# Optimization experiments

Hardware: AMD Instinct MI355X
Metric: run time of the kernel (lower is better)

Reference implementation:

```python
import jax, jax.numpy as jnp
import numpy as np

EPS = 1e-6

def _ln(x, g, b):
    mu = jnp.mean(x, axis=-1, keepdims=True)
    var = jnp.mean(jnp.square(x - mu), axis=-1, keepdims=True)
    return (x - mu) * jax.lax.rsqrt(var + EPS) * g + b

def setup_inputs() -> dict:
    key = jax.random.key(0)
    ks = jax.random.split(key, 8)
    B, S, D, H, HD, F = 4, 1024, 1024, 16, 64, 4096
    s = 0.02
    return {
        "hidden_state": jax.random.normal(ks[0], (B, S, D), jnp.float32),
        "mask": jnp.ones((B, S), jnp.int32),
        "Wq": jax.random.normal(ks[1], (H, D, HD), jnp.float32) * s,
        "bq": jnp.zeros((H, HD), jnp.float32),
        "Wk": jax.random.normal(ks[2], (H, D, HD), jnp.float32) * s,
        "bk": jnp.zeros((H, HD), jnp.float32),
        "Wv": jax.random.normal(ks[3], (H, D, HD), jnp.float32) * s,
        "bv": jnp.zeros((H, HD), jnp.float32),
        "Wo": jax.random.normal(ks[4], (D, D), jnp.float32) * s,
        "bo": jnp.zeros((D,), jnp.float32),
        "ln1_g": jnp.ones((D,), jnp.float32),
        "ln1_b": jnp.zeros((D,), jnp.float32),
        "ln2_g": jnp.ones((D,), jnp.float32),
        "ln2_b": jnp.zeros((D,), jnp.float32),
        "W1": jax.random.normal(ks[5], (D, F), jnp.float32) * s,
        "b1": jnp.zeros((F,), jnp.float32),
        "W2": jax.random.normal(ks[6], (F, D), jnp.float32) * s,
        "b2": jnp.zeros((D,), jnp.float32),
    }

def reference(hidden_state, mask, Wq, bq, Wk, bk, Wv, bv, Wo, bo,
              ln1_g, ln1_b, ln2_g, ln2_b, W1, b1, W2, b2):
    # Pre-norm
    x1 = _ln(hidden_state, ln1_g, ln1_b)  # [B,S,D]
    # Per-head projections stacked over head axis h
    q = jnp.einsum('bsd,hdk->bhsk', x1, Wq) + bq[:, None, :]
    k = jnp.einsum('bsd,hdk->bhsk', x1, Wk) + bk[:, None, :]
    v = jnp.einsum('bsd,hdk->bhsk', x1, Wv) + bv[:, None, :]
    head_dim = q.shape[-1]
    scores = jnp.einsum('bhqk,bhsk->bhqs', q, k) / jnp.sqrt(jnp.float32(head_dim))
    scores = jnp.where(mask[:, None, None, :] == 0, jnp.float32(-1e9), scores)
    w = jax.nn.softmax(scores, axis=-1)
    attn = jnp.einsum('bhqs,bhsk->bhqk', w, v)  # [B,H,S,HD]
    B, H, S, HD = attn.shape
    attn = attn.transpose(0, 2, 1, 3).reshape(B, S, H * HD)  # concat heads
    attn = attn @ Wo + bo
    h = attn + hidden_state
    x2 = _ln(h, ln2_g, ln2_b)
    ff = jax.nn.gelu(x2 @ W1 + b1, approximate=False) @ W2 + b2
    return ff + h
```

## Files before the change

### kernel.cpp

```cpp
#include <hip/hip_runtime.h>

typedef __bf16 bf16;
typedef __bf16 bf16x4 __attribute__((ext_vector_type(4)));
typedef __bf16 bf16x8 __attribute__((ext_vector_type(8)));
typedef float  f32x4  __attribute__((ext_vector_type(4)));

#define F32X4_ZERO ((f32x4){0.f, 0.f, 0.f, 0.f})

__device__ __forceinline__ f32x4 mfma16(bf16x8 a, bf16x8 b, f32x4 c) {
  return __builtin_amdgcn_mfma_f32_16x16x32_bf16(a, b, c, 0, 0, 0);
}

__device__ __forceinline__ void gld16(const void* g, void* l) {
  __builtin_amdgcn_global_load_lds((const __attribute__((address_space(1))) void*)g,
                                   (__attribute__((address_space(3))) void*)l, 16, 0, 0);
}

__device__ __forceinline__ float gelu_f(float u) {
  return 0.5f * u * (1.0f + erff(u * 0.70710678118654752f));
}

__device__ __forceinline__ bf16x8 frag_ld(const bf16* base, int row, int c16) {
  return *(const bf16x8*)((const char*)base + row * 128 + (((c16) ^ (row & 7)) << 4));
}

__device__ __forceinline__ bf16x8 frag_ld32(const bf16* base, int row, int c16) {
  return *(const bf16x8*)((const char*)base + row * 64 + ((c16 ^ ((row >> 1) & 3)) << 4));
}
#define WAITB(N) asm volatile("s_waitcnt vmcnt(" #N ")\ns_barrier" ::: "memory")

__global__ void transpose2(const float* __restrict__ src, size_t sBatch, int sStride,
                           bf16* __restrict__ dst, size_t dBatch, int dStride) {
  __shared__ bf16 t[32][33];
  src += (size_t)blockIdx.z * sBatch;
  dst += (size_t)blockIdx.z * dBatch;
  int c0 = blockIdx.x * 32, r0 = blockIdx.y * 32;
#pragma unroll
  for (int i = 0; i < 4; i++) {
    int r = threadIdx.y + i * 8;
    t[r][threadIdx.x] = (bf16)src[(size_t)(r0 + r) * sStride + c0 + threadIdx.x];
  }
  __syncthreads();
#pragma unroll
  for (int i = 0; i < 4; i++) {
    int c = threadIdx.y + i * 8;
    dst[(size_t)(c0 + c) * dStride + r0 + threadIdx.x] = t[threadIdx.x][c];
  }
}

__global__ __launch_bounds__(256) void ln_rows(const float* __restrict__ in,
                                               const float* __restrict__ gam,
                                               const float* __restrict__ bet,
                                               bf16* __restrict__ out) {
  int row = blockIdx.x, tid = threadIdx.x;
  f32x4 x = *(const f32x4*)(in + (size_t)row * 1024 + tid * 4);
  float s = 0.f, q = 0.f;
#pragma unroll
  for (int j = 0; j < 4; j++) { s += x[j]; q += x[j] * x[j]; }
#pragma unroll
  for (int o = 1; o < 64; o <<= 1) {
    s += __shfl_xor(s, o, 64);
    q += __shfl_xor(q, o, 64);
  }
  __shared__ float red[8];
  if ((tid & 63) == 0) { red[(tid >> 6) * 2] = s; red[(tid >> 6) * 2 + 1] = q; }
  __syncthreads();
  s = red[0] + red[2] + red[4] + red[6];
  q = red[1] + red[3] + red[5] + red[7];
  float mean = s * (1.f / 1024.f);
  float var  = q * (1.f / 1024.f) - mean * mean;
  float inv  = rsqrtf(var + 1e-6f);
  bf16x4 o;
#pragma unroll
  for (int j = 0; j < 4; j++) {
    int c = tid * 4 + j;
    o[j] = (bf16)((x[j] - mean) * inv * gam[c] + bet[c]);
  }
  *(bf16x4*)(out + (size_t)row * 1024 + tid * 4) = o;
}

enum { EPI_WO = 0, EPI_GELU = 1, EPI_ACC0 = 2, EPI_ACC = 3, EPI_FINAL = 4 };

__global__ __launch_bounds__(512) void pipe256x128_gelu(
    const bf16* __restrict__ A, const bf16* __restrict__ BT, const float* __restrict__ bias,
    int N, bf16* __restrict__ outb) {
  int tid = threadIdx.x, lane = tid & 63, wv = tid >> 6;
  int bid = blockIdx.x;
  int xcd = bid & 7, idx = bid >> 3;
  int mg = xcd >> 1, ng = xcd & 1;
  int m0 = (mg * 4 + (idx >> 4)) * 256;
  int n0 = (ng * 16 + (idx & 15)) * 128;
  int wrow = (wv >> 1) * 64, wcol = (wv & 1) * 64;
  __shared__ __align__(16) bf16 lds[3][12288];
  f32x4 acc[4][4];
#pragma unroll
  for (int a = 0; a < 4; a++)
#pragma unroll
    for (int n = 0; n < 4; n++) acc[a][n] = F32X4_ZERO;

  constexpr int K = 1024, nk = K / 32;
  int rin = lane >> 2;
  int sbc = ((lane & 3) ^ ((lane >> 3) & 3)) * 16;
  auto stage = [&](int slot, int k0) {
#pragma unroll
    for (int j = 0; j < 3; j++) {
      int c = wv * 3 + j;
      if (c < 16)
        gld16((const char*)A + ((size_t)(m0 + c * 16 + rin) * K + k0) * 2 + sbc,
              (char*)lds[slot] + c * 1024);
      else
        gld16((const char*)BT + ((size_t)(n0 + (c - 16) * 16 + rin) * K + k0) * 2 + sbc,
              (char*)lds[slot] + c * 1024);
    }
  };

  stage(0, 0); stage(1, 32);
#pragma unroll 1
  for (int t = 0; t < nk; t++) {
    if (t < nk - 1) WAITB(3);
    else            WAITB(0);
    if (t + 2 < nk) stage((t + 2) % 3, (t + 2) * 32);
    const bf16* As = lds[t % 3];
    const bf16* Bs = lds[t % 3] + 8192;
    int c16 = lane >> 4;
    bf16x8 af[4], bfr[4];
#pragma unroll
    for (int mf = 0; mf < 4; mf++)
      af[mf] = frag_ld32(As, wrow + mf * 16 + (lane & 15), c16);
#pragma unroll
    for (int nf = 0; nf < 4; nf++)
      bfr[nf] = frag_ld32(Bs, wcol + nf * 16 + (lane & 15), c16);
#pragma unroll
    for (int mf = 0; mf < 4; mf++)
#pragma unroll
      for (int nf = 0; nf < 4; nf++)
        acc[mf][nf] = mfma16(af[mf], bfr[nf], acc[mf][nf]);
  }
#pragma unroll
  for (int mf = 0; mf < 4; mf++)
#pragma unroll
    for (int nf = 0; nf < 4; nf++)
#pragma unroll
      for (int i = 0; i < 4; i++) {
        int row = m0 + wrow + mf * 16 + ((lane >> 4) << 2) + i;
        int col = n0 + wcol + nf * 16 + (lane & 15);
        outb[(size_t)row * N + col] = (bf16)gelu_f(acc[mf][nf][i] + bias[col]);
      }
}

template <int EPI, int K, int NTL>
__global__ __launch_bounds__(256) void pipe128(
    const bf16* __restrict__ A, const bf16* __restrict__ BT, const float* __restrict__ bias,
    int N,
    const float* __restrict__ resid, float* __restrict__ facc,
    bf16* __restrict__ outb, float* __restrict__ outf) {
  int tid = threadIdx.x, lane = tid & 63, wv = tid >> 6;
  int bid = blockIdx.x + (blockIdx.y << 3);
  int xcd = bid & 7, idx = bid >> 3;
  int m0 = (xcd * 4 + (idx >> NTL)) * 128;
  int n0 = (idx & ((1 << NTL) - 1)) * 128;
  int wrow = (wv >> 1) * 64, wcol = (wv & 1) * 64;
  __shared__ __align__(16) bf16 lds[3][8192];
  f32x4 acc[4][4];
#pragma unroll
  for (int a = 0; a < 4; a++)
#pragma unroll
    for (int n = 0; n < 4; n++) acc[a][n] = F32X4_ZERO;

  constexpr int nk = K / 32;
  int rin = lane >> 2;
  int sbc = ((lane & 3) ^ ((lane >> 3) & 3)) * 16;
  auto stage = [&](int slot, int k0) {
#pragma unroll
    for (int j = 0; j < 4; j++) {
      int c = wv * 4 + j;
      if (c < 8)
        gld16((const char*)A + ((size_t)(m0 + c * 16 + rin) * K + k0) * 2 + sbc,
              (char*)lds[slot] + c * 1024);
      else
        gld16((const char*)BT + ((size_t)(n0 + (c - 8) * 16 + rin) * K + k0) * 2 + sbc,
              (char*)lds[slot] + c * 1024);
    }
  };

  stage(0, 0); stage(1, 32);
#pragma unroll 1
  for (int t = 0; t < nk; t++) {
    if (t < nk - 1) WAITB(4);
    else            WAITB(0);
    if (t + 2 < nk) stage((t + 2) % 3, (t + 2) * 32);
    const bf16* As = lds[t % 3];
    const bf16* Bs = lds[t % 3] + 4096;
    int c16 = lane >> 4;
    bf16x8 af[4], bfr[4];
#pragma unroll
    for (int mf = 0; mf < 4; mf++)
      af[mf] = frag_ld32(As, wrow + mf * 16 + (lane & 15), c16);
#pragma unroll
    for (int nf = 0; nf < 4; nf++)
      bfr[nf] = frag_ld32(Bs, wcol + nf * 16 + (lane & 15), c16);
#pragma unroll
    for (int mf = 0; mf < 4; mf++)
#pragma unroll
      for (int nf = 0; nf < 4; nf++)
        acc[mf][nf] = mfma16(af[mf], bfr[nf], acc[mf][nf]);
  }
#pragma unroll
  for (int mf = 0; mf < 4; mf++)
#pragma unroll
    for (int nf = 0; nf < 4; nf++)
#pragma unroll
      for (int i = 0; i < 4; i++) {
        int row = m0 + wrow + mf * 16 + ((lane >> 4) << 2) + i;
        int col = n0 + wcol + nf * 16 + (lane & 15);
        size_t idx2 = (size_t)row * N + col;
        float v = acc[mf][nf][i];
        if constexpr (EPI == EPI_WO) {
          outf[idx2] = v + bias[col] + resid[idx2];
        } else if constexpr (EPI == EPI_GELU) {
          outb[idx2] = (bf16)gelu_f(v + bias[col]);
        } else if constexpr (EPI == EPI_ACC0) {
          facc[idx2] = v;
        } else if constexpr (EPI == EPI_ACC) {
          facc[idx2] += v;
        } else {
          outf[idx2] = facc[idx2] + v + bias[col] + resid[idx2];
        }
      }
}

template <int KSTRIDE, int KLOOP, int NTL>
__global__ __launch_bounds__(256) void pipe128_part(
    const bf16* __restrict__ Abase, const bf16* __restrict__ BTbase,
    int N, bf16* __restrict__ p0, bf16* __restrict__ p1) {
  int tid = threadIdx.x, lane = tid & 63, wv = tid >> 6;
  int z = blockIdx.z;
  const bf16* A  = Abase  + (size_t)z * KLOOP;
  const bf16* BT = BTbase + (size_t)z * KLOOP;
  bf16* outp = z ? p1 : p0;
  int bid = blockIdx.x + (blockIdx.y << 3);
  int xcd = bid & 7, idx = bid >> 3;
  int m0 = (xcd * 4 + (idx >> NTL)) * 128;
  int n0 = (idx & ((1 << NTL) - 1)) * 128;
  int wrow = (wv >> 1) * 64, wcol = (wv & 1) * 64;
  __shared__ __align__(16) bf16 lds[3][8192];
  f32x4 acc[4][4];
#pragma unroll
  for (int a = 0; a < 4; a++)
#pragma unroll
    for (int n = 0; n < 4; n++) acc[a][n] = F32X4_ZERO;

  constexpr int nk = KLOOP / 32;
  int rin = lane >> 2;
  int sbc = ((lane & 3) ^ ((lane >> 3) & 3)) * 16;
  auto stage = [&](int slot, int k0) {
#pragma unroll
    for (int j = 0; j < 4; j++) {
      int c = wv * 4 + j;
      if (c < 8)
        gld16((const char*)A + ((size_t)(m0 + c * 16 + rin) * KSTRIDE + k0) * 2 + sbc,
              (char*)lds[slot] + c * 1024);
      else
        gld16((const char*)BT + ((size_t)(n0 + (c - 8) * 16 + rin) * KSTRIDE + k0) * 2 + sbc,
              (char*)lds[slot] + c * 1024);
    }
  };

  stage(0, 0); stage(1, 32);
#pragma unroll 1
  for (int t = 0; t < nk; t++) {
    if (t < nk - 1) WAITB(4);
    else            WAITB(0);
    if (t + 2 < nk) stage((t + 2) % 3, (t + 2) * 32);
    const bf16* As = lds[t % 3];
    const bf16* Bs = lds[t % 3] + 4096;
    int c16 = lane >> 4;
    bf16x8 af[4], bfr[4];
#pragma unroll
    for (int mf = 0; mf < 4; mf++)
      af[mf] = frag_ld32(As, wrow + mf * 16 + (lane & 15), c16);
#pragma unroll
    for (int nf = 0; nf < 4; nf++)
      bfr[nf] = frag_ld32(Bs, wcol + nf * 16 + (lane & 15), c16);
#pragma unroll
    for (int mf = 0; mf < 4; mf++)
#pragma unroll
      for (int nf = 0; nf < 4; nf++)
        acc[mf][nf] = mfma16(af[mf], bfr[nf], acc[mf][nf]);
  }
#pragma unroll
  for (int mf = 0; mf < 4; mf++)
#pragma unroll
    for (int nf = 0; nf < 4; nf++)
#pragma unroll
      for (int i = 0; i < 4; i++) {
        int row = m0 + wrow + mf * 16 + ((lane >> 4) << 2) + i;
        int col = n0 + wcol + nf * 16 + (lane & 15);
        outp[(size_t)row * N + col] = (bf16)acc[mf][nf][i];
      }
}

__global__ __launch_bounds__(256) void combine_k(
    const bf16* __restrict__ p0, const bf16* __restrict__ p1,
    const float* __restrict__ bias, const float* __restrict__ resid,
    float* __restrict__ out) {
  size_t i4 = ((size_t)blockIdx.x * 256 + threadIdx.x) * 4;
  bf16x4 a = *(const bf16x4*)(p0 + i4);
  bf16x4 b = *(const bf16x4*)(p1 + i4);
  f32x4 r = *(const f32x4*)(resid + i4);
  f32x4 bb = *(const f32x4*)(bias + (i4 & 1023));
  f32x4 o;
#pragma unroll
  for (int j = 0; j < 4; j++) o[j] = (float)a[j] + (float)b[j] + bb[j] + r[j];
  *(f32x4*)(out + i4) = o;
}

__global__ __launch_bounds__(256) void qkv_pipe(
    const bf16* __restrict__ x1,
    const bf16* __restrict__ WqT, const bf16* __restrict__ WkT, const bf16* __restrict__ WvT,
    const float* __restrict__ bq, const float* __restrict__ bk, const float* __restrict__ bv,
    bf16* __restrict__ qo, bf16* __restrict__ ko, bf16* __restrict__ vto) {
  int tid = threadIdx.x, lane = tid & 63, wv = tid >> 6;
  int z = blockIdx.z;
  const bf16* BT; const float* bias;
  if (z == 0)      { BT = WqT; bias = bq; }
  else if (z == 1) { BT = WkT; bias = bk; }
  else             { BT = WvT; bias = bv; }
  int bid = blockIdx.x + (blockIdx.y << 3);
  int xcd = bid & 7, idx = bid >> 3;
  int m0 = (xcd * 4 + (idx >> 3)) * 128, n0 = (idx & 7) * 128;
  int wrow = (wv >> 1) * 64, wcol = (wv & 1) * 64;
  __shared__ __align__(16) bf16 lds[3][8192];
  f32x4 acc[4][4];
#pragma unroll
  for (int a = 0; a < 4; a++)
#pragma unroll
    for (int n = 0; n < 4; n++) acc[a][n] = F32X4_ZERO;

  constexpr int K = 1024, nk = K / 32;
  int rin = lane >> 2;
  int sbc = ((lane & 3) ^ ((lane >> 3) & 3)) * 16;
  auto stage = [&](int slot, int k0) {
#pragma unroll
    for (int j = 0; j < 4; j++) {
      int c = wv * 4 + j;
      if (c < 8)
        gld16((const char*)x1 + ((size_t)(m0 + c * 16 + rin) * K + k0) * 2 + sbc,
              (char*)lds[slot] + c * 1024);
      else
        gld16((const char*)BT + ((size_t)(n0 + (c - 8) * 16 + rin) * K + k0) * 2 + sbc,
              (char*)lds[slot] + c * 1024);
    }
  };

  stage(0, 0); stage(1, 32);
#pragma unroll 1
  for (int t = 0; t < nk; t++) {
    if (t < nk - 1) WAITB(4);
    else            WAITB(0);
    if (t + 2 < nk) stage((t + 2) % 3, (t + 2) * 32);
    const bf16* As = lds[t % 3];
    const bf16* Bs = lds[t % 3] + 4096;
    int c16 = lane >> 4;
    bf16x8 af[4], bfr[4];
#pragma unroll
    for (int mf = 0; mf < 4; mf++)
      af[mf] = frag_ld32(As, wrow + mf * 16 + (lane & 15), c16);
#pragma unroll
    for (int nf = 0; nf < 4; nf++)
      bfr[nf] = frag_ld32(Bs, wcol + nf * 16 + (lane & 15), c16);
#pragma unroll
    for (int mf = 0; mf < 4; mf++)
#pragma unroll
      for (int nf = 0; nf < 4; nf++)
        acc[mf][nf] = mfma16(af[mf], bfr[nf], acc[mf][nf]);
  }
#pragma unroll
  for (int mf = 0; mf < 4; mf++)
#pragma unroll
    for (int nf = 0; nf < 4; nf++)
#pragma unroll
      for (int i = 0; i < 4; i++) {
        int row  = m0 + wrow + mf * 16 + ((lane >> 4) << 2) + i;
        int ncol = n0 + wcol + nf * 16 + (lane & 15);
        int bb = row >> 10, s = row & 1023, head = ncol >> 6, d = ncol & 63;
        size_t bh = (size_t)bb * 16 + head;
        float v = acc[mf][nf][i] + bias[ncol];
        if (z == 0)      qo[(bh * 1024 + s) * 64 + d] = (bf16)(v * 0.125f);
        else if (z == 1) ko[(bh * 1024 + s) * 64 + d] = (bf16)v;
        else             vto[(bh * 64 + d) * 1024 + s] = (bf16)v;
      }
}

__global__ __launch_bounds__(512) void attn_flash(
    const bf16* __restrict__ qb, const bf16* __restrict__ kb, const bf16* __restrict__ vtb,
    const int* __restrict__ mask, bf16* __restrict__ attnC) {
  int tid = threadIdx.x, lane = tid & 63, wv = tid >> 6;
  int wgid = blockIdx.x;
  int nid  = (wgid & 7) * 64 + (wgid >> 3);
  int qblk = nid & 7, h = (nid >> 3) & 15, b = nid >> 7;
  int qrow0 = qblk * 128 + wv * 16;

  __shared__ float smask[1024];
  __shared__ __align__(16) bf16 kt[2][64 * 64];
  __shared__ __align__(16) bf16 vt[2][64 * 64];
  __shared__ __align__(16) bf16 pb[8][16][72];
  for (int i = tid; i < 1024; i += 512) smask[i] = mask[b * 1024 + i] ? 0.f : -1e9f;

  size_t bh = (size_t)b * 16 + h;
  const bf16* qp = qb + (bh * 1024 + qrow0) * 64;
  bf16x8 qa[2];
#pragma unroll
  for (int kc = 0; kc < 2; kc++)
    qa[kc] = *(const bf16x8*)(qp + (lane & 15) * 64 + kc * 32 + (lane >> 4) * 8);

  const bf16* kp = kb + bh * 1024 * 64;
  const bf16* vp = vtb + bh * 64 * 1024;
  bf16* myp = &pb[wv][0][0];

  bf16x8 vone;
#pragma unroll
  for (int j = 0; j < 8; j++) vone[j] = (bf16)1.0f;

  f32x4 ssum = F32X4_ZERO;
  f32x4 oacc[4];
#pragma unroll
  for (int i = 0; i < 4; i++) oacc[i] = F32X4_ZERO;

  int srl = lane >> 3;
  int sbc = ((lane & 7) ^ srl) * 16;
  auto stage = [&](int buf, int t2) {
    int key0n = t2 * 64;
#pragma unroll
    for (int j = 0; j < 2; j++) {
      int c = wv * 2 + j;
      if (c < 8) {
        int row = c * 8 + srl;
        gld16((const char*)kp + ((size_t)(key0n + row) * 64) * 2 + sbc,
              (char*)kt[buf] + c * 1024);
      } else {
        int row = (c - 8) * 8 + srl;
        gld16((const char*)vp + ((size_t)row * 1024 + key0n) * 2 + sbc,
              (char*)vt[buf] + (c - 8) * 1024);
      }
    }
  };

  stage(0, 0);
  __syncthreads();

  for (int t = 0; t < 16; t++) {
    int cur = t & 1;
    if (t < 15) stage(cur ^ 1, t + 1);
    const bf16* kcur = kt[cur];
    const bf16* vcur = vt[cur];
    int key0 = t * 64;
    f32x4 st[4];
    __builtin_amdgcn_s_setprio(1);
#pragma unroll
    for (int nt = 0; nt < 4; nt++) {
      st[nt] = F32X4_ZERO;
#pragma unroll
      for (int kc = 0; kc < 2; kc++) {
        bf16x8 kf = frag_ld(kcur, nt * 16 + (lane & 15), kc * 4 + (lane >> 4));
        st[nt] = mfma16(qa[kc], kf, st[nt]);
      }
    }
    __builtin_amdgcn_s_setprio(0);
#pragma unroll
    for (int nt = 0; nt < 4; nt++) {
      float ms = smask[key0 + nt * 16 + (lane & 15)] - 8.0f;
#pragma unroll
      for (int i = 0; i < 4; i++) st[nt][i] = __expf(st[nt][i] + ms);
    }
#pragma unroll
    for (int nt = 0; nt < 4; nt++)
#pragma unroll
      for (int i = 0; i < 4; i++)
        myp[((lane >> 4) * 4 + i) * 72 + nt * 16 + (lane & 15)] = (bf16)st[nt][i];
    __builtin_amdgcn_s_setprio(1);
#pragma unroll
    for (int kc = 0; kc < 2; kc++) {
      bf16x8 pa = *(const bf16x8*)(myp + (lane & 15) * 72 + kc * 32 + (lane >> 4) * 8);
      ssum = mfma16(pa, vone, ssum);
#pragma unroll
      for (int dn = 0; dn < 4; dn++) {
        bf16x8 vf = frag_ld(vcur, dn * 16 + (lane & 15), kc * 4 + (lane >> 4));
        oacc[dn] = mfma16(pa, vf, oacc[dn]);
      }
    }
    __builtin_amdgcn_s_setprio(0);
    __syncthreads();
  }
#pragma unroll
  for (int i = 0; i < 4; i++) {
    float inv = 1.0f / ssum[i];
    int row = qrow0 + ((lane >> 4) << 2) + i;
#pragma unroll
    for (int dn = 0; dn < 4; dn++)
      attnC[(size_t)(b * 1024 + row) * 1024 + h * 64 + dn * 16 + (lane & 15)] =
          (bf16)(oacc[dn][i] * inv);
  }
}

template <int EPI, int K>
__global__ __launch_bounds__(256) void gemm_bt(
    const bf16* __restrict__ A, const bf16* __restrict__ BT, const float* __restrict__ bias,
    int N,
    const float* __restrict__ resid, float* __restrict__ facc,
    bf16* __restrict__ outb, float* __restrict__ outf) {
  int tid = threadIdx.x, lane = tid & 63, wv = tid >> 6;
  int m0 = blockIdx.y * 128, n0 = blockIdx.x * 128;
  int wrow = (wv >> 1) * 64, wcol = (wv & 1) * 64;
  __shared__ __align__(16) bf16 lA[2][128 * 64];
  __shared__ __align__(16) bf16 lB[2][128 * 64];
  f32x4 acc[4][4];
#pragma unroll
  for (int a = 0; a < 4; a++)
#pragma unroll
    for (int n = 0; n < 4; n++) acc[a][n] = F32X4_ZERO;

  int cbs = ((lane & 7) ^ (lane >> 3)) * 16;
  auto stage = [&](int buf, int k0) {
#pragma unroll
    for (int s = 0; s < 4; s++) {
      int c = s * 4 + wv;
      int row = c * 8 + (lane >> 3);
      gld16((const char*)A  + ((size_t)(m0 + row) * K + k0) * 2 + cbs,
            (char*)lA[buf] + c * 1024);
      gld16((const char*)BT + ((size_t)(n0 + row) * K + k0) * 2 + cbs,
            (char*)lB[buf] + c * 1024);
    }
  };

  constexpr int nk = K >> 6;
  stage(0, 0);
  __syncthreads();
#pragma unroll 1
  for (int t = 0; t < nk; t++) {
    int cur = t & 1;
    if (t + 1 < nk) stage(cur ^ 1, (t + 1) * 64);
#pragma unroll
    for (int kc = 0; kc < 2; kc++) {
      int c16 = kc * 4 + (lane >> 4);
      bf16x8 af[4], bfr[4];
#pragma unroll
      for (int mf = 0; mf < 4; mf++)
        af[mf] = frag_ld(lA[cur], wrow + mf * 16 + (lane & 15), c16);
#pragma unroll
      for (int nf = 0; nf < 4; nf++)
        bfr[nf] = frag_ld(lB[cur], wcol + nf * 16 + (lane & 15), c16);
#pragma unroll
      for (int mf = 0; mf < 4; mf++)
#pragma unroll
        for (int nf = 0; nf < 4; nf++)
          acc[mf][nf] = mfma16(af[mf], bfr[nf], acc[mf][nf]);
    }
    __syncthreads();
  }
#pragma unroll
  for (int mf = 0; mf < 4; mf++)
#pragma unroll
    for (int nf = 0; nf < 4; nf++)
#pragma unroll
      for (int i = 0; i < 4; i++) {
        int row = m0 + wrow + mf * 16 + ((lane >> 4) << 2) + i;
        int col = n0 + wcol + nf * 16 + (lane & 15);
        size_t idx2 = (size_t)row * N + col;
        float v = acc[mf][nf][i];
        if constexpr (EPI == EPI_WO) {
          outf[idx2] = v + bias[col] + resid[idx2];
        } else if constexpr (EPI == EPI_GELU) {
          outb[idx2] = (bf16)gelu_f(v + bias[col]);
        } else if constexpr (EPI == EPI_ACC0) {
          facc[idx2] = v;
        } else if constexpr (EPI == EPI_ACC) {
          facc[idx2] += v;
        } else {
          outf[idx2] = facc[idx2] + v + bias[col] + resid[idx2];
        }
      }
}

extern "C" void kernel_launch(void* const* d_in, const int* in_sizes, int n_in,
                              void* d_out, int out_size, void* d_ws, size_t ws_size,
                              hipStream_t stream) {
  const float* hidden = (const float*)d_in[0];
  const int*   mask   = (const int*)d_in[1];
  const float* Wq = (const float*)d_in[2];
  const float* bq = (const float*)d_in[3];
  const float* Wk = (const float*)d_in[4];
  const float* bk = (const float*)d_in[5];
  const float* Wv = (const float*)d_in[6];
  const float* bv = (const float*)d_in[7];
  const float* Wo = (const float*)d_in[8];
  const float* bo = (const float*)d_in[9];
  const float* ln1g = (const float*)d_in[10];
  const float* ln1b = (const float*)d_in[11];
  const float* ln2g = (const float*)d_in[12];
  const float* ln2b = (const float*)d_in[13];
  const float* W1 = (const float*)d_in[14];
  const float* b1 = (const float*)d_in[15];
  const float* W2 = (const float*)d_in[16];
  const float* b2 = (const float*)d_in[17];
  float* out = (float*)d_out;

  char* ws = (char*)d_ws;
  const size_t MB = 1ull << 20;
  dim3 tb(32, 8);
  const size_t HB = 64 * 1024;

  if (ws_size >= 96 * MB) {
    bf16* x1    = (bf16*)(ws + 0 * MB);
    bf16* attnC = x1;
    bf16* x2    = x1;
    bf16* part0 = x1;
    bf16* qbuf  = (bf16*)(ws + 8 * MB);
    bf16* W1T   = qbuf;
    bf16* kbuf  = (bf16*)(ws + 16 * MB);
    bf16* W2T   = kbuf;
    bf16* vtbuf = (bf16*)(ws + 24 * MB);
    bf16* part1 = vtbuf;
    float* hbuf = (float*)(ws + 32 * MB);
    bf16* WqT   = (bf16*)(ws + 48 * MB);
    bf16* WkT   = (bf16*)(ws + 50 * MB);
    bf16* WvT   = (bf16*)(ws + 52 * MB);
    bf16* WoT   = (bf16*)(ws + 54 * MB);
    bf16* gbuf  = (bf16*)(ws + 56 * MB);

    transpose2<<<dim3(2, 32, 16), tb, 0, stream>>>(Wq, HB, 64, WqT, HB, 1024);
    transpose2<<<dim3(2, 32, 16), tb, 0, stream>>>(Wk, HB, 64, WkT, HB, 1024);
    transpose2<<<dim3(2, 32, 16), tb, 0, stream>>>(Wv, HB, 64, WvT, HB, 1024);
    transpose2<<<dim3(32, 32, 1), tb, 0, stream>>>(Wo, 0, 1024, WoT, 0, 1024);
    ln_rows<<<4096, 256, 0, stream>>>(hidden, ln1g, ln1b, x1);
    qkv_pipe<<<dim3(8, 32, 3), 256, 0, stream>>>(x1, WqT, WkT, WvT, bq, bk, bv,
                                                 qbuf, kbuf, vtbuf);
    attn_flash<<<512, 512, 0, stream>>>(qbuf, kbuf, vtbuf, mask, attnC);
    pipe128<EPI_WO, 1024, 3><<<dim3(8, 32), 256, 0, stream>>>(attnC, WoT, bo, 1024,
                                                              hidden, nullptr, nullptr, hbuf);
    ln_rows<<<4096, 256, 0, stream>>>(hbuf, ln2g, ln2b, x2);
    transpose2<<<dim3(128, 32, 1), tb, 0, stream>>>(W1, 0, 4096, W1T, 0, 1024);
    transpose2<<<dim3(32, 128, 1), tb, 0, stream>>>(W2, 0, 1024, W2T, 0, 4096);
    pipe256x128_gelu<<<512, 512, 0, stream>>>(x2, W1T, b1, 4096, gbuf);
    pipe128_part<4096, 2048, 3><<<dim3(8, 32, 2), 256, 0, stream>>>(gbuf, W2T, 1024,
                                                                    part0, part1);
    combine_k<<<4096, 256, 0, stream>>>(part0, part1, b2, hbuf, out);
  } else {
    bf16* x1     = (bf16*)(ws + 0 * MB);
    bf16* attnC  = x1;
    bf16* x2     = x1;
    bf16* qbuf   = (bf16*)(ws + 8 * MB);
    bf16* W1Tc   = (bf16*)(ws + 8 * MB);
    bf16* W2Tc   = (bf16*)(ws + 10 * MB);
    bf16* gchunk = (bf16*)(ws + 12 * MB);
    bf16* kbuf   = (bf16*)(ws + 16 * MB);
    bf16* vtbuf  = (bf16*)(ws + 24 * MB);
    float* hbuf  = (float*)(ws + 16 * MB);
    bf16* WqT    = (bf16*)(ws + 32 * MB);
    bf16* WkT    = (bf16*)(ws + 34 * MB);
    bf16* WvT    = (bf16*)(ws + 36 * MB);
    bf16* WoT    = (bf16*)(ws + 38 * MB);
    float* outacc = (float*)(ws + 40 * MB);

    transpose2<<<dim3(2, 32, 16), tb, 0, stream>>>(Wq, HB, 64, WqT, HB, 1024);
    transpose2<<<dim3(2, 32, 16), tb, 0, stream>>>(Wk, HB, 64, WkT, HB, 1024);
    transpose2<<<dim3(2, 32, 16), tb, 0, stream>>>(Wv, HB, 64, WvT, HB, 1024);
    transpose2<<<dim3(32, 32, 1), tb, 0, stream>>>(Wo, 0, 1024, WoT, 0, 1024);
    ln_rows<<<4096, 256, 0, stream>>>(hidden, ln1g, ln1b, x1);
    qkv_pipe<<<dim3(8, 32, 3), 256, 0, stream>>>(x1, WqT, WkT, WvT, bq, bk, bv,
                                                 qbuf, kbuf, vtbuf);
    attn_flash<<<512, 512, 0, stream>>>(qbuf, kbuf, vtbuf, mask, attnC);
    pipe128<EPI_WO, 1024, 3><<<dim3(8, 32), 256, 0, stream>>>(attnC, WoT, bo, 1024,
                                                              hidden, nullptr, nullptr, hbuf);
    ln_rows<<<4096, 256, 0, stream>>>(hbuf, ln2g, ln2b, x2);

    for (int c = 0; c < 8; c++) {
      transpose2<<<dim3(16, 32, 1), tb, 0, stream>>>(W1 + c * 512, 0, 4096,
                                                     W1Tc, 0, 1024);
      transpose2<<<dim3(32, 16, 1), tb, 0, stream>>>(W2 + (size_t)c * 512 * 1024, 0, 1024,
                                                     W2Tc, 0, 512);
      gemm_bt<EPI_GELU, 1024><<<dim3(4, 32), 256, 0, stream>>>(x2, W1Tc, b1 + c * 512, 512,
                                                               nullptr, nullptr, gchunk, nullptr);
      if (c == 0)
        gemm_bt<EPI_ACC0, 512><<<dim3(8, 32), 256, 0, stream>>>(gchunk, W2Tc, b2, 1024,
                                                                nullptr, outacc, nullptr, nullptr);
      else if (c < 7)
        gemm_bt<EPI_ACC, 512><<<dim3(8, 32), 256, 0, stream>>>(gchunk, W2Tc, b2, 1024,
                                                               nullptr, outacc, nullptr, nullptr);
      else
        gemm_bt<EPI_FINAL, 512><<<dim3(8, 32), 256, 0, stream>>>(gchunk, W2Tc, b2, 1024,
                                                                 hbuf, outacc, nullptr, out);
    }
  }

  (void)in_sizes; (void)n_in; (void)out_size;
}
```

Before: 223.1 us.

## Rewrite W1 GEMM as 256x256 tile with 8-phase interleaved load/MFMA pipeline

The FFN up-projection GEMM with fused GELU moves from 256x128 tiles with BK=32 and a triple-buffered LDS pipeline to 256x256 tiles with BK=64, double-buffered, split into four quadrant phases. Each phase loads its fragments, issues the global-to-LDS prefetch for one quarter of the next tile, waits with a tuned vmcnt, and raises wave priority around its MFMA block. The aim is more reuse per tile and finer overlap of memory traffic with MFMA issue. In exchange it doubles accumulator registers, uses 128KB of LDS per block, halves the grid to 256 blocks (fewer than one per CU on some configurations), and adds more barriers per k-step.

Measured after the change: 330.0 us. 47.9% more time.

```diff
diff --git a/kernel.cpp b/kernel.cpp
--- a/kernel.cpp
+++ b/kernel.cpp
@@ -6,6 +6,8 @@
 typedef float  f32x4  __attribute__((ext_vector_type(4)));
 
 #define F32X4_ZERO ((f32x4){0.f, 0.f, 0.f, 0.f})
+
+template <int V> struct IC { static constexpr int v = V; };
 
 __device__ __forceinline__ f32x4 mfma16(bf16x8 a, bf16x8 b, f32x4 c) {
   return __builtin_amdgcn_mfma_f32_16x16x32_bf16(a, b, c, 0, 0, 0);
@@ -81,71 +83,110 @@
 
 enum { EPI_WO = 0, EPI_GELU = 1, EPI_ACC0 = 2, EPI_ACC = 3, EPI_FINAL = 4 };
 
-__global__ __launch_bounds__(512) void pipe256x128_gelu(
+__global__ __launch_bounds__(512) void pipe256_8ph_gelu(
     const bf16* __restrict__ A, const bf16* __restrict__ BT, const float* __restrict__ bias,
     int N, bf16* __restrict__ outb) {
   int tid = threadIdx.x, lane = tid & 63, wv = tid >> 6;
   int bid = blockIdx.x;
   int xcd = bid & 7, idx = bid >> 3;
-  int mg = xcd >> 1, ng = xcd & 1;
-  int m0 = (mg * 4 + (idx >> 4)) * 256;
-  int n0 = (ng * 16 + (idx & 15)) * 128;
-  int wrow = (wv >> 1) * 64, wcol = (wv & 1) * 64;
-  __shared__ __align__(16) bf16 lds[3][12288];
-  f32x4 acc[4][4];
-#pragma unroll
-  for (int a = 0; a < 4; a++)
+  int m0 = ((xcd >> 1) * 4 + (idx >> 3)) * 256;
+  int n0 = ((xcd & 1) * 8 + (idx & 7)) * 256;
+  int wm = wv >> 2, wn = wv & 3;
+  __shared__ __align__(16) bf16 lds[2][32768];
+  f32x4 acc[8][4];
+#pragma unroll
+  for (int a = 0; a < 8; a++)
 #pragma unroll
     for (int n = 0; n < 4; n++) acc[a][n] = F32X4_ZERO;
 
-  constexpr int K = 1024, nk = K / 32;
-  int rin = lane >> 2;
-  int sbc = ((lane & 3) ^ ((lane >> 3) & 3)) * 16;
-  auto stage = [&](int slot, int k0) {
-#pragma unroll
-    for (int j = 0; j < 3; j++) {
-      int c = wv * 3 + j;
-      if (c < 16)
-        gld16((const char*)A + ((size_t)(m0 + c * 16 + rin) * K + k0) * 2 + sbc,
-              (char*)lds[slot] + c * 1024);
-      else
-        gld16((const char*)BT + ((size_t)(n0 + (c - 16) * 16 + rin) * K + k0) * 2 + sbc,
-              (char*)lds[slot] + c * 1024);
-    }
+  constexpr int K = 1024, nt = K / 64;
+  int rin8 = lane >> 3;
+  int cbs  = ((lane & 7) ^ rin8) * 16;
+  int c0   = wv * 2;
+  int r0   = c0 * 8 + rin8;
+  auto stage_half = [&](int slot, int k0, int hid) {
+    const char* s; char* d = (char*)lds[slot] + c0 * 1024;
+    if (hid == 0)      { s = (const char*)A  + ((size_t)(m0 + r0)       * K + k0) * 2 + cbs; }
+    else if (hid == 3) { s = (const char*)A  + ((size_t)(m0 + 128 + r0) * K + k0) * 2 + cbs; d += 16384; }
+    else if (hid == 1) { s = (const char*)BT + ((size_t)(n0 + r0)       * K + k0) * 2 + cbs; d += 32768; }
+    else               { s = (const char*)BT + ((size_t)(n0 + 128 + r0) * K + k0) * 2 + cbs; d += 49152; }
+    gld16(s, d);
+    gld16(s + (size_t)8 * K * 2, d + 1024);
   };
 
-  stage(0, 0); stage(1, 32);
+  stage_half(0, 0, 0); stage_half(0, 0, 1); stage_half(0, 0, 2); stage_half(0, 0, 3);
+  asm volatile("s_waitcnt vmcnt(4)\ns_barrier" ::: "memory");
+
 #pragma unroll 1
-  for (int t = 0; t < nk; t++) {
-    if (t < nk - 1) WAITB(3);
-    else            WAITB(0);
-    if (t + 2 < nk) stage((t + 2) % 3, (t + 2) * 32);
-    const bf16* As = lds[t % 3];
-    const bf16* Bs = lds[t % 3] + 8192;
-    int c16 = lane >> 4;
-    bf16x8 af[4], bfr[4];
+  for (int t = 0; t < nt; t++) {
+    const bf16* bufc = lds[t & 1];
+    int nxt = (t + 1) & 1;
+    int k1 = (t + 1) * 64;
+    bool more = (t + 1 < nt);
+
+    auto phase = [&](auto qc, int hid, int wc) {
+      constexpr int QM = decltype(qc)::v >> 1;
+      constexpr int QN = decltype(qc)::v & 1;
+      bf16x8 af[4][2], bfr[2][2];
+#pragma unroll
+      for (int mf = 0; mf < 4; mf++)
+#pragma unroll
+        for (int kc = 0; kc < 2; kc++)
+          af[mf][kc] = frag_ld(bufc + QM * 8192,
+                               wm * 64 + mf * 16 + (lane & 15), kc * 4 + (lane >> 4));
+#pragma unroll
+      for (int nf = 0; nf < 2; nf++)
+#pragma unroll
+        for (int kc = 0; kc < 2; kc++)
+          bfr[nf][kc] = frag_ld(bufc + 16384 + QN * 8192,
+                                wn * 32 + nf * 16 + (lane & 15), kc * 4 + (lane >> 4));
+      if (more) stage_half(nxt, k1, hid);
+      if (wc == 4)      asm volatile("s_waitcnt vmcnt(4)" ::: "memory");
+      else if (wc == 2) asm volatile("s_waitcnt vmcnt(2)" ::: "memory");
+      else if (wc == 0) asm volatile("s_waitcnt vmcnt(0)" ::: "memory");
+      asm volatile("s_barrier" ::: "memory");
+      __builtin_amdgcn_sched_barrier(0);
+      __builtin_amdgcn_s_setprio(1);
+#pragma unroll
+      for (int mf = 0; mf < 4; mf++)
+#pragma unroll
+        for (int nf = 0; nf < 2; nf++)
+#pragma unroll
+          for (int kc = 0; kc < 2; kc++)
+            acc[QM * 4 + mf][QN * 2 + nf] =
+                mfma16(af[mf][kc], bfr[nf][kc], acc[QM * 4 + mf][QN * 2 + nf]);
+      __builtin_amdgcn_s_setprio(0);
+      asm volatile("s_barrier" ::: "memory");
+    };
+
+    if (more) {
+      phase(IC<0>{}, 0, 4);
+      phase(IC<1>{}, 1, 4);
+      phase(IC<2>{}, 2, -1);
+      phase(IC<3>{}, 3, 4);
+    } else {
+      phase(IC<0>{}, 0, 2);
+      phase(IC<1>{}, 1, 0);
+      phase(IC<2>{}, 2, -1);
+      phase(IC<3>{}, 3, -1);
+    }
+  }
+
+#pragma unroll
+  for (int qm = 0; qm < 2; qm++)
 #pragma unroll
     for (int mf = 0; mf < 4; mf++)
-      af[mf] = frag_ld32(As, wrow + mf * 16 + (lane & 15), c16);
-#pragma unroll
-    for (int nf = 0; nf < 4; nf++)
-      bfr[nf] = frag_ld32(Bs, wcol + nf * 16 + (lane & 15), c16);
-#pragma unroll
-    for (int mf = 0; mf < 4; mf++)
-#pragma unroll
-      for (int nf = 0; nf < 4; nf++)
-        acc[mf][nf] = mfma16(af[mf], bfr[nf], acc[mf][nf]);
-  }
-#pragma unroll
-  for (int mf = 0; mf < 4; mf++)
-#pragma unroll
-    for (int nf = 0; nf < 4; nf++)
-#pragma unroll
-      for (int i = 0; i < 4; i++) {
-        int row = m0 + wrow + mf * 16 + ((lane >> 4) << 2) + i;
-        int col = n0 + wcol + nf * 16 + (lane & 15);
-        outb[(size_t)row * N + col] = (bf16)gelu_f(acc[mf][nf][i] + bias[col]);
-      }
+#pragma unroll
+      for (int qn = 0; qn < 2; qn++)
+#pragma unroll
+        for (int nf = 0; nf < 2; nf++)
+#pragma unroll
+          for (int i = 0; i < 4; i++) {
+            int row = m0 + qm * 128 + wm * 64 + mf * 16 + ((lane >> 4) << 2) + i;
+            int col = n0 + qn * 128 + wn * 32 + nf * 16 + (lane & 15);
+            outb[(size_t)row * N + col] =
+                (bf16)gelu_f(acc[qm * 4 + mf][qn * 2 + nf][i] + bias[col]);
+          }
 }
 
 template <int EPI, int K, int NTL>
@@ -641,7 +682,7 @@
     ln_rows<<<4096, 256, 0, stream>>>(hbuf, ln2g, ln2b, x2);
     transpose2<<<dim3(128, 32, 1), tb, 0, stream>>>(W1, 0, 4096, W1T, 0, 1024);
     transpose2<<<dim3(32, 128, 1), tb, 0, stream>>>(W2, 0, 1024, W2T, 0, 4096);
-    pipe256x128_gelu<<<512, 512, 0, stream>>>(x2, W1T, b1, 4096, gbuf);
+    pipe256_8ph_gelu<<<256, 512, 0, stream>>>(x2, W1T, b1, 4096, gbuf);
     pipe128_part<4096, 2048, 3><<<dim3(8, 32, 2), 256, 0, stream>>>(gbuf, W2T, 1024,
                                                                     part0, part1);
     combine_k<<<4096, 256, 0, stream>>>(part0, part1, b2, hbuf, out);
```
